# Kernel tuning notes

Hardware: AMD Instinct MI355X
Metric: run time of the kernel (lower is better)

The kernel has to match this reference:

```python
import jax, jax.numpy as jnp
import numpy as np

DIM = 768
HEADS = 12
DIM_HEAD = DIM // HEADS
FACTOR = DIM_HEAD ** (-0.5)
B, T = 4, 2048


def setup_inputs() -> dict:
    key = jax.random.key(0)
    k1, k2, k3 = jax.random.split(key, 3)
    x = jax.random.normal(k1, (B, T, DIM), dtype=jnp.float32)
    # VarianceScaling-like init scale for linear weights
    W_qkv = jax.random.normal(k2, (DIM, 3 * DIM), dtype=jnp.float32) * (DIM ** -0.5)
    W_out = jax.random.normal(k3, (DIM, DIM), dtype=jnp.float32) * (DIM ** -0.5)
    return {"x": x, "W_qkv": W_qkv, "W_out": W_out}


def reference(x, W_qkv, W_out):
    b, t, _ = x.shape
    qkv = x @ W_qkv  # [b, t, 3*dim]
    # einops 'b t (d k h) -> k b h t d' with k=3, h=HEADS: d slowest, k middle, h fastest
    qkv = qkv.reshape(b, t, DIM_HEAD, 3, HEADS)
    qkv = jnp.transpose(qkv, (3, 0, 4, 1, 2))  # [3, b, h, t, d]
    q, k, v = qkv[0], qkv[1], qkv[2]
    # scaled dot-product attention, full [b,h,t,t] scores as in the original
    scores = jnp.einsum('bhid,bhjd->bhij', q, k) * FACTOR
    attn = jax.nn.softmax(scores, axis=-1)
    out = jnp.einsum('bhij,bhjd->bhid', attn, v)  # [b, h, t, d]
    # 'b h t d -> b t (h d)'
    out = jnp.transpose(out, (0, 2, 1, 3)).reshape(b, t, HEADS * DIM_HEAD)
    return out @ W_out
```

## Files before the change

kernel.cpp:

```cpp
#include <hip/hip_runtime.h>
#include <hip/hip_bf16.h>

#define DIM    768
#define HEADS  12
#define DHEAD  64
#define BATCH  4
#define SEQ    2048
#define NROW   (BATCH * SEQ)
#define QKVN   (3 * DIM)
#define FACTOR 0.125f
#define QSCALE 0.18033688011112042f

typedef __attribute__((ext_vector_type(8))) short short8;
typedef __attribute__((ext_vector_type(4))) float floatx4;

__device__ __forceinline__ floatx4 mfma16(short8 a, short8 b, floatx4 c) {
    return __builtin_amdgcn_mfma_f32_16x16x32_bf16(a, b, c, 0, 0, 0);
}

__device__ __forceinline__ short rne16(float f) {
    unsigned u = __builtin_bit_cast(unsigned, f);
    return (short)((u + 0x7fffu + ((u >> 16) & 1u)) >> 16);
}
__device__ __forceinline__ unsigned pack2(float lo, float hi) {
    unsigned ul = __builtin_bit_cast(unsigned, lo);
    unsigned uh = __builtin_bit_cast(unsigned, hi);
    ul = (ul + 0x7fffu + ((ul >> 16) & 1u)) >> 16;
    uh = (uh + 0x7fffu + ((uh >> 16) & 1u)) & 0xffff0000u;
    return ul | uh;
}

__device__ __forceinline__ int swz8(int row, int col) {
    return (row << 6) + ((((col >> 3) ^ row) & 7) << 3) + (col & 7);
}

__global__ __launch_bounds__(256) void conv_bf16(const float* __restrict__ x,
                                                 short* __restrict__ xb) {
    int g = blockIdx.x * 256 + threadIdx.x;
    float4 v = ((const float4*)x)[g];
    uint2 o;
    o.x = pack2(v.x, v.y);
    o.y = pack2(v.z, v.w);
    ((uint2*)xb)[g] = o;
}

__global__ __launch_bounds__(256) void transpose_w(const float* __restrict__ W,
                                                   short* __restrict__ Wt,
                                                   int K, int N, int permute) {
    __shared__ short T[32][33];
    int n0 = blockIdx.x * 32, k0 = blockIdx.y * 32;
    int c = threadIdx.x & 31, r0 = threadIdx.x >> 5;
    for (int r = r0; r < 32; r += 8)
        T[r][c] = rne16(W[(size_t)(k0 + r) * N + n0 + c]);
    __syncthreads();
    for (int r = r0; r < 32; r += 8) {
        int n = n0 + r;
        int np;
        if (permute) {
            int d = n / 36, rem = n - d * 36;
            int which = rem / 12, h = rem - which * 12;
            np = which * 768 + h * 64 + d;
        } else {
            np = n;
        }
        Wt[(size_t)np * K + k0 + c] = T[c][r];
    }
}

__global__ __launch_bounds__(256) void gemm_qkv(const short* __restrict__ A,
                                                const short* __restrict__ Bt,
                                                short* __restrict__ Qo,
                                                short* __restrict__ Ko,
                                                short* __restrict__ Vto) {
    __shared__ short As[128 * 64];
    __shared__ short Bs[128 * 64];
    const int tid = threadIdx.x;
    const int lane = tid & 63, wave = tid >> 6;
    const int l15 = lane & 15, quad = lane >> 4;

    const int flat = blockIdx.x;
    const int xcd = flat & 7;
    const int local = flat >> 3;
    const int mloc = local & 7, nloc = local >> 3;
    const int m0 = (xcd * 8 + mloc) * 128;
    const int n0 = nloc * 128;

    const int wm = (wave >> 1) * 64, wn = (wave & 1) * 64;

    floatx4 acc[4][4] = {};
    for (int k0 = 0; k0 < DIM; k0 += 64) {
#pragma unroll
        for (int i = 0; i < 4; ++i) {
            int idx = tid + i * 256;
            int row = idx >> 3, c = idx & 7;
            int loff = (row << 6) + (((c ^ row) & 7) << 3);
            *(uint4*)&As[loff] = *(const uint4*)&A[(size_t)(m0 + row) * DIM + k0 + c * 8];
            *(uint4*)&Bs[loff] = *(const uint4*)&Bt[(size_t)(n0 + row) * DIM + k0 + c * 8];
        }
        __syncthreads();
#pragma unroll
        for (int ks = 0; ks < 2; ++ks) {
            short8 a[4], b[4];
#pragma unroll
            for (int mt = 0; mt < 4; ++mt)
                a[mt] = *(const short8*)&As[swz8(wm + mt * 16 + l15, ks * 32 + quad * 8)];
#pragma unroll
            for (int nt = 0; nt < 4; ++nt)
                b[nt] = *(const short8*)&Bs[swz8(wn + nt * 16 + l15, ks * 32 + quad * 8)];
#pragma unroll
            for (int mt = 0; mt < 4; ++mt)
#pragma unroll
                for (int nt = 0; nt < 4; ++nt)
                    acc[mt][nt] = mfma16(a[mt], b[nt], acc[mt][nt]);
        }
        __syncthreads();
    }

    const int sn = n0 + wn;
    const int which = sn / 768;
    const int h = (sn - which * 768) >> 6;
    const int bb = (m0 + wm) >> 11;
    const int tbase = (m0 + wm) & 2047;

    if (which != 2) {
        short* dst = (which == 0) ? Qo : Ko;
        const float scale = (which == 0) ? QSCALE : 1.0f;
        const size_t rowbase = ((size_t)(bb * HEADS + h) * SEQ + tbase) * DHEAD;
#pragma unroll
        for (int mt = 0; mt < 4; ++mt)
#pragma unroll
            for (int nt = 0; nt < 4; ++nt) {
                int d = nt * 16 + l15;
#pragma unroll
                for (int r = 0; r < 4; ++r) {
                    int tl = mt * 16 + quad * 4 + r;
                    dst[rowbase + (size_t)tl * DHEAD + d] = rne16(acc[mt][nt][r] * scale);
                }
            }
    } else {
        short* vld = ((wave < 2) ? As : Bs) + (wave & 1) * 4096;
#pragma unroll
        for (int mt = 0; mt < 4; ++mt)
#pragma unroll
            for (int nt = 0; nt < 4; ++nt) {
                int d = nt * 16 + l15;
                int tl = mt * 16 + quad * 4;
                int chunk = (tl >> 3) ^ (d & 7);
                int addr = (d << 6) + (chunk << 3) + (tl & 7);
                uint2 pk;
                pk.x = pack2(acc[mt][nt][0], acc[mt][nt][1]);
                pk.y = pack2(acc[mt][nt][2], acc[mt][nt][3]);
                *(uint2*)&vld[addr] = pk;
            }
    }
    __syncthreads();
    if (which == 2) {
        short* vld = ((wave < 2) ? As : Bs) + (wave & 1) * 4096;
        const size_t vbase = ((size_t)(bb * HEADS + h) * DHEAD) * SEQ;
#pragma unroll
        for (int i = 0; i < 8; ++i) {
            int c = lane + i * 64;
            int d = c >> 3, j = c & 7;
            int addr = (d << 6) + (((j ^ (d & 7)) & 7) << 3);
            uint4 v = *(const uint4*)&vld[addr];
            *(uint4*)&Vto[vbase + (size_t)d * SEQ + tbase + j * 8] = v;
        }
    }
}

__global__ __launch_bounds__(512, 6) void attn_mfma(const short* __restrict__ Q,
                                                    const short* __restrict__ K,
                                                    const short* __restrict__ Vt,
                                                    short* __restrict__ O) {
    __shared__ short lds[128 * 64];
    __shared__ short Ps[8 * 16 * 64];

    const int tid = threadIdx.x;
    const int lane = tid & 63, wave = tid >> 6;
    const int l15 = lane & 15, quad = lane >> 4;
    const int bh = blockIdx.y;
    const int q0 = blockIdx.x * 128;
    const size_t base = (size_t)bh * SEQ * DHEAD;
    const int wr = wave * 16;
    short* myP = Ps + wave * (16 * 64);
    short* Ks = lds;
    short* Vs = lds + 4096;

#pragma unroll
    for (int i = 0; i < 2; ++i) {
        int idx = tid + i * 512;
        int row = idx >> 3, c = idx & 7;
        *(uint4*)&lds[(row << 6) + (((c ^ row) & 7) << 3)] =
            *(const uint4*)&Q[base + (size_t)(q0 + row) * DHEAD + c * 8];
    }
    __syncthreads();
    short8 qf[2];
#pragma unroll
    for (int ks = 0; ks < 2; ++ks)
        qf[ks] = *(const short8*)&lds[swz8(wr + l15, ks * 32 + quad * 8)];
    __syncthreads();

    floatx4 o[4] = {};
    float lsum = 0.f;

    for (int j0 = 0; j0 < SEQ; j0 += 64) {
        {
            int row = tid >> 3, c = tid & 7;
            int loff = (row << 6) + (((c ^ row) & 7) << 3);
            *(uint4*)&Ks[loff] = *(const uint4*)&K[base + (size_t)(j0 + row) * DHEAD + c * 8];
            *(uint4*)&Vs[loff] = *(const uint4*)&Vt[base + (size_t)row * SEQ + j0 + c * 8];
        }
        __syncthreads();

        floatx4 s[4] = {};
#pragma unroll
        for (int ks = 0; ks < 2; ++ks) {
            short8 kf[4];
#pragma unroll
            for (int kt = 0; kt < 4; ++kt)
                kf[kt] = *(const short8*)&Ks[swz8(kt * 16 + l15, ks * 32 + quad * 8)];
#pragma unroll
            for (int kt = 0; kt < 4; ++kt)
                s[kt] = mfma16(kf[kt], qf[ks], s[kt]);
        }

#pragma unroll
        for (int kt = 0; kt < 4; ++kt) {
            float p0 = __builtin_amdgcn_exp2f(s[kt][0]);
            float p1 = __builtin_amdgcn_exp2f(s[kt][1]);
            float p2 = __builtin_amdgcn_exp2f(s[kt][2]);
            float p3 = __builtin_amdgcn_exp2f(s[kt][3]);
            lsum += (p0 + p1) + (p2 + p3);
            uint2 pk;
            pk.x = pack2(p0, p1);
            pk.y = pack2(p2, p3);
            *(uint2*)&myP[swz8(l15, kt * 16 + quad * 4)] = pk;
        }

#pragma unroll
        for (int ks = 0; ks < 2; ++ks) {
            short8 a = *(const short8*)&myP[swz8(l15, ks * 32 + quad * 8)];
            short8 b[4];
#pragma unroll
            for (int dt = 0; dt < 4; ++dt)
                b[dt] = *(const short8*)&Vs[swz8(dt * 16 + l15, ks * 32 + quad * 8)];
#pragma unroll
            for (int dt = 0; dt < 4; ++dt)
                o[dt] = mfma16(a, b[dt], o[dt]);
        }
        __syncthreads();
    }

    const int b = bh / HEADS, h = bh - b * HEADS;
    float rs = lsum;
    rs += __shfl_xor(rs, 16);
    rs += __shfl_xor(rs, 32);
    float invl = 1.f / rs;
#pragma unroll
    for (int r = 0; r < 4; ++r) {
        float inv = __shfl(invl, quad * 4 + r);
        int t = q0 + wr + quad * 4 + r;
#pragma unroll
        for (int dt = 0; dt < 4; ++dt) {
            int d = dt * 16 + l15;
            O[((size_t)(b * SEQ + t)) * DIM + h * DHEAD + d] = rne16(o[dt][r] * inv);
        }
    }
}

__global__ __launch_bounds__(256) void gemm_out(const short* __restrict__ A,
                                                const short* __restrict__ Bt,
                                                float* __restrict__ out) {
    __shared__ short As[128 * 64];
    __shared__ short Bs[128 * 64];
    const int tid = threadIdx.x;
    const int lane = tid & 63, wave = tid >> 6;
    const int l15 = lane & 15, quad = lane >> 4;
    const int m0 = blockIdx.y * 128, n0 = blockIdx.x * 128;
    const int wm = (wave >> 1) * 64, wn = (wave & 1) * 64;

    floatx4 acc[4][4] = {};
    for (int k0 = 0; k0 < DIM; k0 += 64) {
#pragma unroll
        for (int i = 0; i < 4; ++i) {
            int idx = tid + i * 256;
            int row = idx >> 3, c = idx & 7;
            int loff = (row << 6) + (((c ^ row) & 7) << 3);
            *(uint4*)&As[loff] = *(const uint4*)&A[(size_t)(m0 + row) * DIM + k0 + c * 8];
            *(uint4*)&Bs[loff] = *(const uint4*)&Bt[(size_t)(n0 + row) * DIM + k0 + c * 8];
        }
        __syncthreads();
#pragma unroll
        for (int ks = 0; ks < 2; ++ks) {
            short8 a[4], b[4];
#pragma unroll
            for (int mt = 0; mt < 4; ++mt)
                a[mt] = *(const short8*)&As[swz8(wm + mt * 16 + l15, ks * 32 + quad * 8)];
#pragma unroll
            for (int nt = 0; nt < 4; ++nt)
                b[nt] = *(const short8*)&Bs[swz8(wn + nt * 16 + l15, ks * 32 + quad * 8)];
#pragma unroll
            for (int mt = 0; mt < 4; ++mt)
#pragma unroll
                for (int nt = 0; nt < 4; ++nt)
                    acc[mt][nt] = mfma16(a[mt], b[nt], acc[mt][nt]);
        }
        __syncthreads();
    }

#pragma unroll
    for (int mt = 0; mt < 4; ++mt)
#pragma unroll
        for (int nt = 0; nt < 4; ++nt)
#pragma unroll
            for (int r = 0; r < 4; ++r) {
                int m = m0 + wm + mt * 16 + quad * 4 + r;
                int n = n0 + wn + nt * 16 + l15;
                out[(size_t)m * DIM + n] = acc[mt][nt][r];
            }
}

extern "C" void kernel_launch(void* const* d_in, const int* in_sizes, int n_in,
                              void* d_out, int out_size, void* d_ws, size_t ws_size,
                              hipStream_t stream) {
    const float* x    = (const float*)d_in[0];
    const float* Wqkv = (const float*)d_in[1];
    const float* Wout = (const float*)d_in[2];
    float* out = (float*)d_out;

    const size_t NE = (size_t)NROW * DIM;
    short* xb  = (short*)d_ws;
    short* Wqt = xb + NE;
    short* Wot = Wqt + (size_t)QKVN * DIM;
    short* Qw  = Wot + (size_t)DIM * DIM;
    short* Kw  = Qw + NE;
    short* Vtw = Kw + NE;

    conv_bf16<<<NE / 4 / 256, 256, 0, stream>>>(x, xb);
    transpose_w<<<dim3(QKVN / 32, DIM / 32), 256, 0, stream>>>(Wqkv, Wqt, DIM, QKVN, 1);
    transpose_w<<<dim3(DIM / 32, DIM / 32), 256, 0, stream>>>(Wout, Wot, DIM, DIM, 0);
    gemm_qkv<<<8 * 8 * 18, 256, 0, stream>>>(xb, Wqt, Qw, Kw, Vtw);
    attn_mfma<<<dim3(SEQ / 128, BATCH * HEADS), 512, 0, stream>>>(Qw, Kw, Vtw, xb);
    gemm_out<<<dim3(DIM / 128, NROW / 128), 256, 0, stream>>>(xb, Wot, out);
}
```

Measured before the change: 237.0 us.

## Use 32x32 MFMA with split-KV waves and direct global-to-LDS loads

Tile loads in all three kernels now go straight from global memory into LDS through global_load_lds, with the XOR swizzle applied on the source address instead of staging through registers. The attention kernel switches to 32x32x16 bf16 MFMA. Each pair of waves shares 32 query rows and splits every 64-key tile into two halves, and the partial outputs and row sums are merged through LDS at the end. The intent is to cut register staging and VGPR traffic and raise MFMA efficiency, at the cost of a cross-wave reduction and a larger shared-memory footprint.

```diff
diff --git a/kernel.cpp b/kernel.cpp
--- a/kernel.cpp
+++ b/kernel.cpp
@@ -13,9 +13,19 @@
 
 typedef __attribute__((ext_vector_type(8))) short short8;
 typedef __attribute__((ext_vector_type(4))) float floatx4;
+typedef __attribute__((ext_vector_type(16))) float floatx16;
 
 __device__ __forceinline__ floatx4 mfma16(short8 a, short8 b, floatx4 c) {
     return __builtin_amdgcn_mfma_f32_16x16x32_bf16(a, b, c, 0, 0, 0);
+}
+__device__ __forceinline__ floatx16 mfma32(short8 a, short8 b, floatx16 c) {
+    return __builtin_amdgcn_mfma_f32_32x32x16_bf16(a, b, c, 0, 0, 0);
+}
+
+__device__ __forceinline__ void glds16(const void* g, void* l) {
+    __builtin_amdgcn_global_load_lds((const __attribute__((address_space(1))) void*)g,
+                                     (__attribute__((address_space(3))) void*)l,
+                                     16, 0, 0);
 }
 
 __device__ __forceinline__ short rne16(float f) {
@@ -86,16 +96,17 @@
     const int n0 = nloc * 128;
 
     const int wm = (wave >> 1) * 64, wn = (wave & 1) * 64;
+    const int r8 = wave * 8 + (lane >> 3);
+    const int c8 = lane & 7;
+    const int sc = ((c8 ^ (r8 & 7)) << 3);
 
     floatx4 acc[4][4] = {};
     for (int k0 = 0; k0 < DIM; k0 += 64) {
 #pragma unroll
         for (int i = 0; i < 4; ++i) {
-            int idx = tid + i * 256;
-            int row = idx >> 3, c = idx & 7;
-            int loff = (row << 6) + (((c ^ row) & 7) << 3);
-            *(uint4*)&As[loff] = *(const uint4*)&A[(size_t)(m0 + row) * DIM + k0 + c * 8];
-            *(uint4*)&Bs[loff] = *(const uint4*)&Bt[(size_t)(n0 + row) * DIM + k0 + c * 8];
+            int row = i * 32 + r8;
+            glds16(&A[(size_t)(m0 + row) * DIM + k0 + sc], &As[(size_t)(i * 32 + wave * 8) * 64]);
+            glds16(&Bt[(size_t)(n0 + row) * DIM + k0 + sc], &Bs[(size_t)(i * 32 + wave * 8) * 64]);
         }
         __syncthreads();
 #pragma unroll
@@ -172,98 +183,105 @@
                                                     const short* __restrict__ K,
                                                     const short* __restrict__ Vt,
                                                     short* __restrict__ O) {
-    __shared__ short lds[128 * 64];
-    __shared__ short Ps[8 * 16 * 64];
+    __shared__ __align__(16) short buf[17408];
 
     const int tid = threadIdx.x;
     const int lane = tid & 63, wave = tid >> 6;
-    const int l15 = lane & 15, quad = lane >> 4;
+    const int l31 = lane & 31, hi = lane >> 5;
+    const int pair = wave >> 1, kvh = wave & 1;
     const int bh = blockIdx.y;
     const int q0 = blockIdx.x * 128;
     const size_t base = (size_t)bh * SEQ * DHEAD;
-    const int wr = wave * 16;
-    short* myP = Ps + wave * (16 * 64);
-    short* Ks = lds;
-    short* Vs = lds + 4096;
-
+    short* Ks = buf;
+    short* Vs = buf + 4096;
+    short* myP = buf + 8192 + wave * 1024;
+
+    const int srow = wave * 8 + (lane >> 3);
+    const int ssc = (((lane & 7) ^ (srow & 7)) << 3);
 #pragma unroll
     for (int i = 0; i < 2; ++i) {
-        int idx = tid + i * 512;
-        int row = idx >> 3, c = idx & 7;
-        *(uint4*)&lds[(row << 6) + (((c ^ row) & 7) << 3)] =
-            *(const uint4*)&Q[base + (size_t)(q0 + row) * DHEAD + c * 8];
-    }
-    __syncthreads();
-    short8 qf[2];
-#pragma unroll
-    for (int ks = 0; ks < 2; ++ks)
-        qf[ks] = *(const short8*)&lds[swz8(wr + l15, ks * 32 + quad * 8)];
-    __syncthreads();
-
-    floatx4 o[4] = {};
+        int row = i * 64 + srow;
+        glds16(&Q[base + (size_t)(q0 + row) * DHEAD + ssc],
+               &buf[(size_t)(i * 64 + wave * 8) * 64]);
+    }
+    __syncthreads();
+    short8 qf[4];
+#pragma unroll
+    for (int s = 0; s < 4; ++s)
+        qf[s] = *(const short8*)&buf[swz8(pair * 32 + l31, s * 16 + hi * 8)];
+    __syncthreads();
+
+    floatx16 o0 = {}, o1 = {};
     float lsum = 0.f;
 
+    int pw[4];
+#pragma unroll
+    for (int g = 0; g < 4; ++g)
+        pw[g] = l31 * 32 + ((g ^ (l31 & 3)) << 3) + 4 * hi;
+    const int pr0 = l31 * 32 + (((hi) ^ (l31 & 3)) << 3);
+    const int pr1 = l31 * 32 + (((2 + hi) ^ (l31 & 3)) << 3);
+
     for (int j0 = 0; j0 < SEQ; j0 += 64) {
-        {
-            int row = tid >> 3, c = tid & 7;
-            int loff = (row << 6) + (((c ^ row) & 7) << 3);
-            *(uint4*)&Ks[loff] = *(const uint4*)&K[base + (size_t)(j0 + row) * DHEAD + c * 8];
-            *(uint4*)&Vs[loff] = *(const uint4*)&Vt[base + (size_t)row * SEQ + j0 + c * 8];
-        }
-        __syncthreads();
-
-        floatx4 s[4] = {};
-#pragma unroll
-        for (int ks = 0; ks < 2; ++ks) {
-            short8 kf[4];
-#pragma unroll
-            for (int kt = 0; kt < 4; ++kt)
-                kf[kt] = *(const short8*)&Ks[swz8(kt * 16 + l15, ks * 32 + quad * 8)];
-#pragma unroll
-            for (int kt = 0; kt < 4; ++kt)
-                s[kt] = mfma16(kf[kt], qf[ks], s[kt]);
-        }
-
-#pragma unroll
-        for (int kt = 0; kt < 4; ++kt) {
-            float p0 = __builtin_amdgcn_exp2f(s[kt][0]);
-            float p1 = __builtin_amdgcn_exp2f(s[kt][1]);
-            float p2 = __builtin_amdgcn_exp2f(s[kt][2]);
-            float p3 = __builtin_amdgcn_exp2f(s[kt][3]);
+        glds16(&K[base + (size_t)(j0 + srow) * DHEAD + ssc], &Ks[(size_t)(wave * 8) * 64]);
+        glds16(&Vt[base + (size_t)srow * SEQ + j0 + ssc], &Vs[(size_t)(wave * 8) * 64]);
+        __syncthreads();
+
+        floatx16 s = {};
+#pragma unroll
+        for (int st = 0; st < 4; ++st) {
+            short8 kf = *(const short8*)&Ks[swz8(kvh * 32 + l31, st * 16 + hi * 8)];
+            s = mfma32(kf, qf[st], s);
+        }
+
+#pragma unroll
+        for (int g = 0; g < 4; ++g) {
+            float p0 = __builtin_amdgcn_exp2f(s[4 * g + 0]);
+            float p1 = __builtin_amdgcn_exp2f(s[4 * g + 1]);
+            float p2 = __builtin_amdgcn_exp2f(s[4 * g + 2]);
+            float p3 = __builtin_amdgcn_exp2f(s[4 * g + 3]);
             lsum += (p0 + p1) + (p2 + p3);
             uint2 pk;
             pk.x = pack2(p0, p1);
             pk.y = pack2(p2, p3);
-            *(uint2*)&myP[swz8(l15, kt * 16 + quad * 4)] = pk;
-        }
-
-#pragma unroll
-        for (int ks = 0; ks < 2; ++ks) {
-            short8 a = *(const short8*)&myP[swz8(l15, ks * 32 + quad * 8)];
-            short8 b[4];
-#pragma unroll
-            for (int dt = 0; dt < 4; ++dt)
-                b[dt] = *(const short8*)&Vs[swz8(dt * 16 + l15, ks * 32 + quad * 8)];
-#pragma unroll
-            for (int dt = 0; dt < 4; ++dt)
-                o[dt] = mfma16(a, b[dt], o[dt]);
-        }
-        __syncthreads();
-    }
-
-    const int b = bh / HEADS, h = bh - b * HEADS;
-    float rs = lsum;
-    rs += __shfl_xor(rs, 16);
-    rs += __shfl_xor(rs, 32);
-    float invl = 1.f / rs;
-#pragma unroll
-    for (int r = 0; r < 4; ++r) {
-        float inv = __shfl(invl, quad * 4 + r);
-        int t = q0 + wr + quad * 4 + r;
-#pragma unroll
-        for (int dt = 0; dt < 4; ++dt) {
-            int d = dt * 16 + l15;
-            O[((size_t)(b * SEQ + t)) * DIM + h * DHEAD + d] = rne16(o[dt][r] * inv);
+            *(uint2*)&myP[pw[g]] = pk;
+        }
+
+#pragma unroll
+        for (int s2 = 0; s2 < 2; ++s2) {
+            short8 a = *(const short8*)&myP[s2 ? pr1 : pr0];
+            short8 b0 = *(const short8*)&Vs[swz8(l31, kvh * 32 + s2 * 16 + hi * 8)];
+            short8 b1 = *(const short8*)&Vs[swz8(32 + l31, kvh * 32 + s2 * 16 + hi * 8)];
+            o0 = mfma32(a, b0, o0);
+            o1 = mfma32(a, b1, o1);
+        }
+        __syncthreads();
+    }
+
+    float rs = lsum + __shfl_xor(lsum, 32);
+    float* Om = (float*)buf;
+    float* Lx = (float*)(buf + 16384);
+    if (wave & 1) {
+        Lx[pair * 32 + l31] = rs;
+#pragma unroll
+        for (int r = 0; r < 16; ++r) {
+            Om[pair * 2048 + r * 64 + hi * 32 + l31] = o0[r];
+            Om[pair * 2048 + (16 + r) * 64 + hi * 32 + l31] = o1[r];
+        }
+    }
+    __syncthreads();
+    if (!(wave & 1)) {
+        const int b = bh / HEADS, h = bh - b * HEADS;
+        float inv = 1.f / (rs + Lx[pair * 32 + l31]);
+        Lx[pair * 32 + l31] = inv;
+#pragma unroll
+        for (int r = 0; r < 16; ++r) {
+            int qr = (r & 3) + 8 * (r >> 2) + 4 * hi;
+            float invr = Lx[pair * 32 + qr];
+            float v0 = o0[r] + Om[pair * 2048 + r * 64 + hi * 32 + l31];
+            float v1 = o1[r] + Om[pair * 2048 + (16 + r) * 64 + hi * 32 + l31];
+            size_t rowo = ((size_t)(b * SEQ + q0 + pair * 32 + qr)) * DIM + h * 64;
+            O[rowo + l31] = rne16(v0 * invr);
+            O[rowo + 32 + l31] = rne16(v1 * invr);
         }
     }
 }
@@ -278,16 +296,16 @@
     const int l15 = lane & 15, quad = lane >> 4;
     const int m0 = blockIdx.y * 128, n0 = blockIdx.x * 128;
     const int wm = (wave >> 1) * 64, wn = (wave & 1) * 64;
+    const int r8 = wave * 8 + (lane >> 3);
+    const int sc = (((lane & 7) ^ (r8 & 7)) << 3);
 
     floatx4 acc[4][4] = {};
     for (int k0 = 0; k0 < DIM; k0 += 64) {
 #pragma unroll
         for (int i = 0; i < 4; ++i) {
-            int idx = tid + i * 256;
-            int row = idx >> 3, c = idx & 7;
-            int loff = (row << 6) + (((c ^ row) & 7) << 3);
-            *(uint4*)&As[loff] = *(const uint4*)&A[(size_t)(m0 + row) * DIM + k0 + c * 8];
-            *(uint4*)&Bs[loff] = *(const uint4*)&Bt[(size_t)(n0 + row) * DIM + k0 + c * 8];
+            int row = i * 32 + r8;
+            glds16(&A[(size_t)(m0 + row) * DIM + k0 + sc], &As[(size_t)(i * 32 + wave * 8) * 64]);
+            glds16(&Bt[(size_t)(n0 + row) * DIM + k0 + sc], &Bs[(size_t)(i * 32 + wave * 8) * 64]);
         }
         __syncthreads();
 #pragma unroll
```

New measurement: 283.2 us. +19.5%, slower.

## Use direct global-to-LDS loads with pre-swizzled tiled Q/K/V layout and XCD-aware attention grid

Applied to the files above, without the earlier changes.

Replaces the register-staged global-to-LDS copies in both GEMMs and the attention kernel with global_load_lds 16-byte transfers. The QKV GEMM now writes Q, K and V^T in pre-swizzled 64x64 tiles, so the attention kernel can copy contiguous tiles straight into LDS without recomputing addresses. The attention grid is flattened and remapped so blocks sharing a batch-head land on the same XCD for L2 reuse. The aim is to cut VGPR pressure and load-issue overhead. In exchange, the layout contract between the kernels is tighter, and scattered element-wise Q/K stores still remain.

```diff
diff --git a/kernel.cpp b/kernel.cpp
--- a/kernel.cpp
+++ b/kernel.cpp
@@ -16,6 +16,12 @@
 
 __device__ __forceinline__ floatx4 mfma16(short8 a, short8 b, floatx4 c) {
     return __builtin_amdgcn_mfma_f32_16x16x32_bf16(a, b, c, 0, 0, 0);
+}
+
+__device__ __forceinline__ void glds16(const void* g, void* l) {
+    __builtin_amdgcn_global_load_lds((const __attribute__((address_space(1))) void*)g,
+                                     (__attribute__((address_space(3))) void*)l,
+                                     16, 0, 0);
 }
 
 __device__ __forceinline__ short rne16(float f) {
@@ -86,16 +92,17 @@
     const int n0 = nloc * 128;
 
     const int wm = (wave >> 1) * 64, wn = (wave & 1) * 64;
+    const int r8 = wave * 8 + (lane >> 3);
+    const int c8 = lane & 7;
+    const int sc = ((c8 ^ (r8 & 7)) << 3);
 
     floatx4 acc[4][4] = {};
     for (int k0 = 0; k0 < DIM; k0 += 64) {
 #pragma unroll
         for (int i = 0; i < 4; ++i) {
-            int idx = tid + i * 256;
-            int row = idx >> 3, c = idx & 7;
-            int loff = (row << 6) + (((c ^ row) & 7) << 3);
-            *(uint4*)&As[loff] = *(const uint4*)&A[(size_t)(m0 + row) * DIM + k0 + c * 8];
-            *(uint4*)&Bs[loff] = *(const uint4*)&Bt[(size_t)(n0 + row) * DIM + k0 + c * 8];
+            int row = i * 32 + r8;
+            glds16(&A[(size_t)(m0 + row) * DIM + k0 + sc], &As[(size_t)(i * 32 + wave * 8) * 64]);
+            glds16(&Bt[(size_t)(n0 + row) * DIM + k0 + sc], &Bs[(size_t)(i * 32 + wave * 8) * 64]);
         }
         __syncthreads();
 #pragma unroll
@@ -121,11 +128,11 @@
     const int h = (sn - which * 768) >> 6;
     const int bb = (m0 + wm) >> 11;
     const int tbase = (m0 + wm) & 2047;
+    const size_t tilebase = ((size_t)(bb * HEADS + h) * 32 + (tbase >> 6)) * 4096;
 
     if (which != 2) {
         short* dst = (which == 0) ? Qo : Ko;
         const float scale = (which == 0) ? QSCALE : 1.0f;
-        const size_t rowbase = ((size_t)(bb * HEADS + h) * SEQ + tbase) * DHEAD;
 #pragma unroll
         for (int mt = 0; mt < 4; ++mt)
 #pragma unroll
@@ -134,7 +141,7 @@
 #pragma unroll
                 for (int r = 0; r < 4; ++r) {
                     int tl = mt * 16 + quad * 4 + r;
-                    dst[rowbase + (size_t)tl * DHEAD + d] = rne16(acc[mt][nt][r] * scale);
+                    dst[tilebase + swz8(tl, d)] = rne16(acc[mt][nt][r] * scale);
                 }
             }
     } else {
@@ -156,14 +163,10 @@
     __syncthreads();
     if (which == 2) {
         short* vld = ((wave < 2) ? As : Bs) + (wave & 1) * 4096;
-        const size_t vbase = ((size_t)(bb * HEADS + h) * DHEAD) * SEQ;
 #pragma unroll
         for (int i = 0; i < 8; ++i) {
-            int c = lane + i * 64;
-            int d = c >> 3, j = c & 7;
-            int addr = (d << 6) + (((j ^ (d & 7)) & 7) << 3);
-            uint4 v = *(const uint4*)&vld[addr];
-            *(uint4*)&Vto[vbase + (size_t)d * SEQ + tbase + j * 8] = v;
+            int c = (i * 64 + lane) * 8;
+            *(uint4*)&Vto[tilebase + c] = *(const uint4*)&vld[c];
         }
     }
 }
@@ -172,44 +175,44 @@
                                                     const short* __restrict__ K,
                                                     const short* __restrict__ Vt,
                                                     short* __restrict__ O) {
-    __shared__ short lds[128 * 64];
-    __shared__ short Ps[8 * 16 * 64];
+    __shared__ __align__(16) short buf[8192];
+    __shared__ __align__(16) short Ps[8192];
 
     const int tid = threadIdx.x;
     const int lane = tid & 63, wave = tid >> 6;
     const int l15 = lane & 15, quad = lane >> 4;
-    const int bh = blockIdx.y;
-    const int q0 = blockIdx.x * 128;
+    const int flat = blockIdx.x;
+    const int xcd = flat & 7, li = flat >> 3;
+    const int bh = xcd + (li % 6) * 8;
+    const int q0 = (li / 6) * 128;
     const size_t base = (size_t)bh * SEQ * DHEAD;
     const int wr = wave * 16;
-    short* myP = Ps + wave * (16 * 64);
-    short* Ks = lds;
-    short* Vs = lds + 4096;
-
-#pragma unroll
-    for (int i = 0; i < 2; ++i) {
-        int idx = tid + i * 512;
-        int row = idx >> 3, c = idx & 7;
-        *(uint4*)&lds[(row << 6) + (((c ^ row) & 7) << 3)] =
-            *(const uint4*)&Q[base + (size_t)(q0 + row) * DHEAD + c * 8];
+    short* myP = Ps + wave * 1024;
+    short* Ks = buf;
+    short* Vs = buf + 4096;
+    const int lane8 = lane * 8;
+
+    {
+        size_t qtb = base + (size_t)(q0 >> 6) * 4096;
+#pragma unroll
+        for (int i = 0; i < 2; ++i)
+            glds16(&Q[qtb + (size_t)(i * 8 + wave) * 512 + lane8],
+                   &buf[(i * 8 + wave) * 512]);
     }
     __syncthreads();
     short8 qf[2];
 #pragma unroll
     for (int ks = 0; ks < 2; ++ks)
-        qf[ks] = *(const short8*)&lds[swz8(wr + l15, ks * 32 + quad * 8)];
+        qf[ks] = *(const short8*)&buf[swz8(wr + l15, ks * 32 + quad * 8)];
     __syncthreads();
 
     floatx4 o[4] = {};
     float lsum = 0.f;
 
     for (int j0 = 0; j0 < SEQ; j0 += 64) {
-        {
-            int row = tid >> 3, c = tid & 7;
-            int loff = (row << 6) + (((c ^ row) & 7) << 3);
-            *(uint4*)&Ks[loff] = *(const uint4*)&K[base + (size_t)(j0 + row) * DHEAD + c * 8];
-            *(uint4*)&Vs[loff] = *(const uint4*)&Vt[base + (size_t)row * SEQ + j0 + c * 8];
-        }
+        size_t ktb = base + (size_t)(j0 >> 6) * 4096 + wave * 512 + lane8;
+        glds16(&K[ktb], &Ks[wave * 512]);
+        glds16(&Vt[ktb], &Vs[wave * 512]);
         __syncthreads();
 
         floatx4 s[4] = {};
@@ -278,16 +281,16 @@
     const int l15 = lane & 15, quad = lane >> 4;
     const int m0 = blockIdx.y * 128, n0 = blockIdx.x * 128;
     const int wm = (wave >> 1) * 64, wn = (wave & 1) * 64;
+    const int r8 = wave * 8 + (lane >> 3);
+    const int sc = (((lane & 7) ^ (r8 & 7)) << 3);
 
     floatx4 acc[4][4] = {};
     for (int k0 = 0; k0 < DIM; k0 += 64) {
 #pragma unroll
         for (int i = 0; i < 4; ++i) {
-            int idx = tid + i * 256;
-            int row = idx >> 3, c = idx & 7;
-            int loff = (row << 6) + (((c ^ row) & 7) << 3);
-            *(uint4*)&As[loff] = *(const uint4*)&A[(size_t)(m0 + row) * DIM + k0 + c * 8];
-            *(uint4*)&Bs[loff] = *(const uint4*)&Bt[(size_t)(n0 + row) * DIM + k0 + c * 8];
+            int row = i * 32 + r8;
+            glds16(&A[(size_t)(m0 + row) * DIM + k0 + sc], &As[(size_t)(i * 32 + wave * 8) * 64]);
+            glds16(&Bt[(size_t)(n0 + row) * DIM + k0 + sc], &Bs[(size_t)(i * 32 + wave * 8) * 64]);
         }
         __syncthreads();
 #pragma unroll
@@ -340,6 +343,6 @@
     transpose_w<<<dim3(QKVN / 32, DIM / 32), 256, 0, stream>>>(Wqkv, Wqt, DIM, QKVN, 1);
     transpose_w<<<dim3(DIM / 32, DIM / 32), 256, 0, stream>>>(Wout, Wot, DIM, DIM, 0);
     gemm_qkv<<<8 * 8 * 18, 256, 0, stream>>>(xb, Wqt, Qw, Kw, Vtw);
-    attn_mfma<<<dim3(SEQ / 128, BATCH * HEADS), 512, 0, stream>>>(Qw, Kw, Vtw, xb);
+    attn_mfma<<<768, 512, 0, stream>>>(Qw, Kw, Vtw, xb);
     gemm_out<<<dim3(DIM / 128, NROW / 128), 256, 0, stream>>>(xb, Wot, out);
 }
```

Result: faster. 225.6 us (-4.8%).
